# Kernel optimization log

Measured on AMD Instinct MI355X. Metric: run time of the kernel, lower is better.

Reference implementation:

```python
import jax, jax.numpy as jnp
import numpy as np

B, N_ANG, LX, LY, LZ = 2, 120, 128, 128, 128


def _rotate_z(vol, phi):
    """Rotate vol [B,Lx,Ly,Lz] by phi radians (counterclockwise) in the (x,y)
    plane about the grid center, bilinear interpolation, zero padding.
    Mirrors pytomography's rotate_detector_z (bilinear grid-sample rotate)."""
    Lx, Ly = vol.shape[1], vol.shape[2]
    dt = vol.dtype
    cx = (Lx - 1) / 2.0
    cy = (Ly - 1) / 2.0
    xs = jnp.arange(Lx, dtype=dt) - cx
    ys = jnp.arange(Ly, dtype=dt) - cy
    X, Y = jnp.meshgrid(xs, ys, indexing="ij")  # [Lx,Ly]
    c, s = jnp.cos(phi), jnp.sin(phi)
    # inverse rotation maps each output pixel to its source location
    sx = c * X + s * Y + cx
    sy = -s * X + c * Y + cy
    x0 = jnp.floor(sx)
    y0 = jnp.floor(sy)
    wx = (sx - x0)[None, :, :, None]
    wy = (sy - y0)[None, :, :, None]
    x0i = x0.astype(jnp.int32)
    y0i = y0.astype(jnp.int32)

    def gather(xi, yi):
        valid = (xi >= 0) & (xi < Lx) & (yi >= 0) & (yi < Ly)
        xic = jnp.clip(xi, 0, Lx - 1)
        yic = jnp.clip(yi, 0, Ly - 1)
        v = vol[:, xic, yic, :]  # [B,Lx,Ly,Lz]
        return v * valid.astype(dt)[None, :, :, None]

    v00 = gather(x0i, y0i)
    v01 = gather(x0i, y0i + 1)
    v10 = gather(x0i + 1, y0i)
    v11 = gather(x0i + 1, y0i + 1)
    return (v00 * (1 - wx) * (1 - wy) + v01 * (1 - wx) * wy
            + v10 * wx * (1 - wy) + v11 * wx * wy)


def setup_inputs() -> dict:
    key = jax.random.key(0)
    image = jax.random.uniform(key, (B, N_ANG, LY, LZ), dtype=jnp.float32)
    angles = jnp.linspace(0.0, 360.0, N_ANG, endpoint=False).astype(jnp.float32)
    return {"image": image, "angles": angles}


def reference(image, angles, delta=1e-11):
    # image: [B, N_angles, Lr, Lz]; angles in degrees.
    Bn, Na, Lr, Lz = image.shape
    Lx = Ly = Lr
    dt = image.dtype
    phis = -jnp.deg2rad(angles).astype(dt)  # negative=True -> back-rotation

    def step(carry, inp):
        obj_acc, norm_acc = carry
        proj, phi = inp  # proj: [B, Lr, Lz]
        # image[:, i].unsqueeze(1) * ones([B, Lx, Ly, Lz]): broadcast along x
        obj_i = jnp.broadcast_to(proj[:, None, :, :], (Bn, Lx, Ly, Lz))
        norm_i = jnp.ones((Bn, Lx, Ly, Lz), dt)
        obj_acc = obj_acc + _rotate_z(obj_i, phi)
        norm_acc = norm_acc + _rotate_z(norm_i, phi)
        return (obj_acc, norm_acc), None

    init = (jnp.zeros((Bn, Lx, Ly, Lz), dt), jnp.zeros((Bn, Lx, Ly, Lz), dt))
    (obj, norm), _ = jax.lax.scan(step, init, (jnp.swapaxes(image, 0, 1), phis))
    return obj / (norm + jnp.asarray(delta, dt))
```

## Files before the change

kernel.cpp:

```cpp
#include <hip/hip_runtime.h>

namespace {

constexpr int L     = 128;
constexpr int NANG  = 120;
constexpr int CHUNK = 60;
constexpr size_t H16_BYTES = (size_t)2 * NANG * L * L * 2;

typedef __fp16 f16x2 __attribute__((ext_vector_type(2)));
typedef __fp16 f16x4 __attribute__((ext_vector_type(4)));
typedef float  f32x4 __attribute__((ext_vector_type(4)));

__global__ __launch_bounds__(256) void cvt16_kernel(const float* __restrict__ in,
                                                    unsigned* __restrict__ out) {
    const int i = ((int)blockIdx.x * 256 + (int)threadIdx.x) * 4;
    const float4 v = *reinterpret_cast<const float4*>(in + i);
    f16x2 a = __builtin_amdgcn_cvt_pkrtz(v.x, v.y);
    f16x2 b = __builtin_amdgcn_cvt_pkrtz(v.z, v.w);
    uint2 st;
    st.x = *reinterpret_cast<unsigned*>(&a);
    st.y = *reinterpret_cast<unsigned*>(&b);
    *reinterpret_cast<uint2*>(out + i / 2) = st;
}

template <bool F16>
__global__ __launch_bounds__(1024, 4) void bp_kernel(
    const void* __restrict__ imgv,
    const float* __restrict__ angles,
    float* __restrict__ out)
{
    constexpr unsigned SLICE = F16 ? 32768u : 65536u;
    constexpr unsigned ROWB  = F16 ? 256u  : 512u;
    constexpr int      RSH   = F16 ? 8 : 9;

    __shared__ unsigned long long aftab[CHUNK * 4 * 64];
    __shared__ float2   acs[NANG];
    __shared__ unsigned arloB[NANG];
    __shared__ alignas(16) float nrmtab[64];

    const int tid = threadIdx.x;
    const int bid = (int)blockIdx.x;
    const int n   = ((bid & 7) << 5) | (bid >> 3);
    int xt = 0, yt = 0;
#pragma unroll
    for (int i = 0; i < 4; ++i) {
        xt |= ((n >> (2 * i)) & 1) << i;
        yt |= ((n >> (2 * i + 1)) & 1) << i;
    }
    const int xb = xt * 8, yb = yt * 8;
    const float cx = (L - 1) * 0.5f;

    if (tid < NANG) {
        const float phi = -angles[tid] * 0.017453292519943295f;
        float s, c;
        sincosf(phi, &s, &c);
        const float X0 = (float)xb - cx,  X1 = (float)(xb + 7) - cx;
        const float Y0 = (float)yb - cx,  Y1 = (float)(yb + 7) - cx;
        const float a00 = -s * X0 + c * Y0 + cx;
        const float a01 = -s * X0 + c * Y1 + cx;
        const float a10 = -s * X1 + c * Y0 + cx;
        const float a11 = -s * X1 + c * Y1 + cx;
        const float symin = fminf(fminf(a00, a01), fminf(a10, a11));
        acs[tid]   = make_float2(c, s);
        arloB[tid] = (unsigned)min(max((int)floorf(symin), 0), 116) << RSH;
    }
    if (tid < 64) nrmtab[tid] = 0.f;
    __syncthreads();

    const int wave  = tid >> 6;
    const int lane  = tid & 63;
    const int quad  = lane >> 4;
    const int lhalf = lane & 15;
    const int zq    = wave & 3;
    const int b     = (wave >> 2) & 1;
    const int aset  = wave >> 3;
    const char* __restrict__ imgc = (const char*)imgv;

    const unsigned bbase_s = __builtin_amdgcn_readfirstlane((unsigned)(b * NANG) * SLICE);
    const unsigned voffc = (unsigned)((quad == 3) ? 0 : quad) * 4u * ROWB
                         + (unsigned)(zq * 32 + 2 * lhalf) * (F16 ? 2u : 4u);

    auto fill_chunk = [&](int c) {
#pragma unroll
        for (int k = 0; k < 15; ++k) {
            const int e  = tid + k * 1024;
            const int ln = e & 63;
            const int m  = (e >> 6) & 3;
            const int ia = e >> 8;
            const int a  = c * CHUNK + ia;
            const int p  = m * 16 + (ln & 15);
            const int qd = ln >> 4;
            const float2 cs = acs[a];
            const int rlo = (int)(arloB[a] >> RSH);
            const float X = (float)(xb + (p >> 3)) - cx;
            const float Y = (float)(yb + (p & 7)) - cx;
            const float sx =  cs.x * X + cs.y * Y + cx;
            const float sy = -cs.y * X + cs.x * Y + cx;
            const float x0f = floorf(sx), y0f = floorf(sy);
            const float wx = sx - x0f,    wy = sy - y0f;
            const int x0 = (int)x0f, y0 = (int)y0f;
            const float mx0 = (x0 >= 0  && x0 <  L)     ? 1.f : 0.f;
            const float mx1 = (x0 >= -1 && x0 <= L - 2) ? 1.f : 0.f;
            const float my0 = (y0 >= 0  && y0 <  L)     ? 1.f : 0.f;
            const float my1 = (y0 >= -1 && y0 <= L - 2) ? 1.f : 0.f;
            const float A   = (1.f - wx) * mx0 + wx * mx1;
            float w0f = (1.f - wy) * my0 * A;
            float w1f = wy * my1 * A;
            const int y0c = min(max(y0, 0), L - 1);
            const int y1c = min(max(y0 + 1, 0), L - 1);
            const int s0  = min(max(y0c - rlo, 0), 11);
            const int s1  = min(max(y1c - rlo, 0), 11);
            if (s0 == s1) { w0f += w1f; w1f = 0.f; }
            f16x2 wh = __builtin_amdgcn_cvt_pkrtz(w0f, w1f);
            const unsigned wbits = *reinterpret_cast<unsigned*>(&wh);
            const unsigned t  = (unsigned)s0 & 3u;
            const int      q0 = s0 >> 2;
            const unsigned long long W = (unsigned long long)wbits << (t * 16u);
            const unsigned long long spill =
                (t == 3u) ? (unsigned long long)(wbits >> 16) : 0ull;
            aftab[e] = (qd == q0) ? W : ((qd == q0 + 1) ? spill : 0ull);
            if (qd == 0) atomicAdd(&nrmtab[p], w0f + w1f);
        }
    };

    f32x4 acc[4][2] = {};

    auto issue = [&](unsigned long long* af, unsigned* r, float2* rf,
                     int i, int c) {
        const int ia = aset + 2 * i;
        const int a  = c * CHUNK + ia;
#pragma unroll
        for (int m = 0; m < 4; ++m)
            af[m] = aftab[ia * 256 + m * 64 + lane];
        const unsigned rlB = __builtin_amdgcn_readfirstlane(arloB[a]);
        const char* pa = imgc + (bbase_s + (unsigned)a * SLICE + rlB);
        if constexpr (F16) {
#pragma unroll
            for (int j = 0; j < 4; ++j)
                r[j] = *(const unsigned*)(pa + (voffc + (unsigned)j * ROWB));
        } else {
#pragma unroll
            for (int j = 0; j < 4; ++j)
                rf[j] = *(const float2*)(pa + (voffc + (unsigned)j * ROWB));
        }
    };
    auto compute = [&](const unsigned long long* af, const unsigned* r,
                       const float2* rf) {
        union { unsigned u[2]; f16x4 v; } B0, B1;
        if constexpr (F16) {
            B0.u[0] = __builtin_amdgcn_perm(r[1], r[0], 0x05040100u);
            B0.u[1] = __builtin_amdgcn_perm(r[3], r[2], 0x05040100u);
            B1.u[0] = __builtin_amdgcn_perm(r[1], r[0], 0x07060302u);
            B1.u[1] = __builtin_amdgcn_perm(r[3], r[2], 0x07060302u);
        } else {
            const f16x2 h0a = __builtin_amdgcn_cvt_pkrtz(rf[0].x, rf[1].x);
            const f16x2 h0b = __builtin_amdgcn_cvt_pkrtz(rf[2].x, rf[3].x);
            const f16x2 h1a = __builtin_amdgcn_cvt_pkrtz(rf[0].y, rf[1].y);
            const f16x2 h1b = __builtin_amdgcn_cvt_pkrtz(rf[2].y, rf[3].y);
            B0.v = f16x4{h0a.x, h0a.y, h0b.x, h0b.y};
            B1.v = f16x4{h1a.x, h1a.y, h1b.x, h1b.y};
        }
#pragma unroll
        for (int m = 0; m < 4; ++m) {
            union { unsigned long long u; f16x4 v; } afu; afu.u = af[m];
            acc[m][0] = __builtin_amdgcn_mfma_f32_16x16x16f16(afu.v, B0.v, acc[m][0], 0, 0, 0);
            acc[m][1] = __builtin_amdgcn_mfma_f32_16x16x16f16(afu.v, B1.v, acc[m][1], 0, 0, 0);
        }
    };

    unsigned long long aA[4], aB[4], aC[4];
    unsigned rA[4], rB[4], rC[4];
    float2   fA[4], fB[4], fC[4];

    for (int c = 0; c < 2; ++c) {
        fill_chunk(c);
        __syncthreads();
        issue(aA, rA, fA, 0, c);
        issue(aB, rB, fB, 1, c);
        for (int i = 0; i < 30; i += 3) {
            if (i + 2 < 30) issue(aC, rC, fC, i + 2, c);
            compute(aA, rA, fA);
            if (i + 3 < 30) issue(aA, rA, fA, i + 3, c);
            compute(aB, rB, fB);
            if (i + 4 < 30) issue(aB, rB, fB, i + 4, c);
            compute(aC, rC, fC);
            __builtin_amdgcn_s_barrier();
        }
        __syncthreads();
    }

    float4* red = reinterpret_cast<float4*>(aftab);
    const int pr = wave & 7;
    if (aset == 1) {
#pragma unroll
        for (int m = 0; m < 4; ++m)
#pragma unroll
            for (int zg = 0; zg < 2; ++zg)
                red[(pr * 8 + m * 2 + zg) * 64 + lane] =
                    make_float4(acc[m][zg][0], acc[m][zg][1],
                                acc[m][zg][2], acc[m][zg][3]);
    }
    __syncthreads();
    if (aset == 0) {
#pragma unroll
        for (int m = 0; m < 4; ++m)
#pragma unroll
            for (int zg = 0; zg < 2; ++zg) {
                const float4 o = red[(pr * 8 + m * 2 + zg) * 64 + lane];
                acc[m][zg][0] += o.x; acc[m][zg][1] += o.y;
                acc[m][zg][2] += o.z; acc[m][zg][3] += o.w;
            }
        const int zb = zq * 32 + 2 * lhalf;
#pragma unroll
        for (int m = 0; m < 4; ++m) {
            const float4 nrm4 = *(const float4*)&nrmtab[m * 16 + quad * 4];
            const float iv[4] = { 1.f / (nrm4.x + 1e-11f), 1.f / (nrm4.y + 1e-11f),
                                  1.f / (nrm4.z + 1e-11f), 1.f / (nrm4.w + 1e-11f) };
#pragma unroll
            for (int r = 0; r < 4; ++r) {
                const int p = m * 16 + quad * 4 + r;
                const int x = xb + (p >> 3);
                const int y = yb + (p & 7);
                const float2 o = make_float2(acc[m][0][r] * iv[r],
                                             acc[m][1][r] * iv[r]);
                *reinterpret_cast<float2*>(
                    &out[(((size_t)(b * L + x)) * L + y) * L + zb]) = o;
            }
        }
    }
}

}

extern "C" void kernel_launch(void* const* d_in, const int* in_sizes, int n_in,
                              void* d_out, int out_size, void* d_ws, size_t ws_size,
                              hipStream_t stream) {
    const float* image  = (const float*)d_in[0];
    const float* angles = (const float*)d_in[1];
    float* out = (float*)d_out;
    (void)in_sizes; (void)n_in; (void)out_size;

    dim3 grid(256);
    if (d_ws != nullptr && ws_size >= H16_BYTES) {
        cvt16_kernel<<<dim3(3840), 256, 0, stream>>>(image, (unsigned*)d_ws);
        bp_kernel<true><<<grid, 1024, 0, stream>>>(d_ws, angles, out);
    } else {
        bp_kernel<false><<<grid, 1024, 0, stream>>>(image, angles, out);
    }
}
```

Baseline: 115.0 us.

## Split z across blocks, halve per-wave M tiles, shrink angle chunks for occupancy

Doubles the grid to 512 blocks by splitting the z dimension into two halves per block. Within a block the waves now split the M (pixel) tiles in half, so each wave holds half as many accumulators. The angle-weight LDS table is filled in chunks of 24 angles over 5 passes instead of 60 over 2, which shrinks shared memory and allows launch bounds of 8 waves per SIMD. The per-iteration s_barrier is also dropped. The trade-off is that weight-table fill and angle trig are duplicated across the two z halves, and there are more chunk syncs.

Measured after the change: 122.5 us. 6.5% more time.

```diff
diff --git a/kernel.cpp b/kernel.cpp
--- a/kernel.cpp
+++ b/kernel.cpp
@@ -4,7 +4,7 @@
 
 constexpr int L     = 128;
 constexpr int NANG  = 120;
-constexpr int CHUNK = 60;
+constexpr int CHUNK = 24;
 constexpr size_t H16_BYTES = (size_t)2 * NANG * L * L * 2;
 
 typedef __fp16 f16x2 __attribute__((ext_vector_type(2)));
@@ -24,7 +24,7 @@
 }
 
 template <bool F16>
-__global__ __launch_bounds__(1024, 4) void bp_kernel(
+__global__ __launch_bounds__(1024, 8) void bp_kernel(
     const void* __restrict__ imgv,
     const float* __restrict__ angles,
     float* __restrict__ out)
@@ -39,13 +39,15 @@
     __shared__ alignas(16) float nrmtab[64];
 
     const int tid = threadIdx.x;
-    const int bid = (int)blockIdx.x;
-    const int n   = ((bid & 7) << 5) | (bid >> 3);
+    const int bid  = (int)blockIdx.x;
+    const int n    = ((bid & 7) << 6) | (bid >> 3);
+    const int zhf  = n & 1;
+    const int tt   = n >> 1;
     int xt = 0, yt = 0;
 #pragma unroll
     for (int i = 0; i < 4; ++i) {
-        xt |= ((n >> (2 * i)) & 1) << i;
-        yt |= ((n >> (2 * i + 1)) & 1) << i;
+        xt |= ((tt >> (2 * i)) & 1) << i;
+        yt |= ((tt >> (2 * i + 1)) & 1) << i;
     }
     const int xb = xt * 8, yb = yt * 8;
     const float cx = (L - 1) * 0.5f;
@@ -71,25 +73,21 @@
     const int lane  = tid & 63;
     const int quad  = lane >> 4;
     const int lhalf = lane & 15;
-    const int zq    = wave & 3;
-    const int b     = (wave >> 2) & 1;
-    const int aset  = wave >> 3;
+    const int zq2   = wave & 1;
+    const int b     = (wave >> 1) & 1;
+    const int aset  = (wave >> 2) & 1;
+    const int mhalf = wave >> 3;
     const char* __restrict__ imgc = (const char*)imgv;
 
     const unsigned bbase_s = __builtin_amdgcn_readfirstlane((unsigned)(b * NANG) * SLICE);
     const unsigned voffc = (unsigned)((quad == 3) ? 0 : quad) * 4u * ROWB
-                         + (unsigned)(zq * 32 + 2 * lhalf) * (F16 ? 2u : 4u);
+        + (unsigned)(zhf * 64 + zq2 * 32 + 2 * lhalf) * (F16 ? 2u : 4u);
 
     auto fill_chunk = [&](int c) {
-#pragma unroll
-        for (int k = 0; k < 15; ++k) {
-            const int e  = tid + k * 1024;
-            const int ln = e & 63;
-            const int m  = (e >> 6) & 3;
-            const int ia = e >> 8;
+        for (int e = tid; e < CHUNK * 64; e += 1024) {
+            const int p  = e & 63;
+            const int ia = e >> 6;
             const int a  = c * CHUNK + ia;
-            const int p  = m * 16 + (ln & 15);
-            const int qd = ln >> 4;
             const float2 cs = acs[a];
             const int rlo = (int)(arloB[a] >> RSH);
             const float X = (float)(xb + (p >> 3)) - cx;
@@ -118,20 +116,24 @@
             const unsigned long long W = (unsigned long long)wbits << (t * 16u);
             const unsigned long long spill =
                 (t == 3u) ? (unsigned long long)(wbits >> 16) : 0ull;
-            aftab[e] = (qd == q0) ? W : ((qd == q0 + 1) ? spill : 0ull);
-            if (qd == 0) atomicAdd(&nrmtab[p], w0f + w1f);
+            const int eb = ia * 256 + (p >> 4) * 64 + (p & 15);
+#pragma unroll
+            for (int qd = 0; qd < 4; ++qd)
+                aftab[eb + qd * 16] =
+                    (qd == q0) ? W : ((qd == q0 + 1) ? spill : 0ull);
+            atomicAdd(&nrmtab[p], w0f + w1f);
         }
     };
 
-    f32x4 acc[4][2] = {};
+    f32x4 acc[2][2] = {};
 
     auto issue = [&](unsigned long long* af, unsigned* r, float2* rf,
                      int i, int c) {
         const int ia = aset + 2 * i;
         const int a  = c * CHUNK + ia;
 #pragma unroll
-        for (int m = 0; m < 4; ++m)
-            af[m] = aftab[ia * 256 + m * 64 + lane];
+        for (int m = 0; m < 2; ++m)
+            af[m] = aftab[ia * 256 + (mhalf * 2 + m) * 64 + lane];
         const unsigned rlB = __builtin_amdgcn_readfirstlane(arloB[a]);
         const char* pa = imgc + (bbase_s + (unsigned)a * SLICE + rlB);
         if constexpr (F16) {
@@ -161,64 +163,64 @@
             B1.v = f16x4{h1a.x, h1a.y, h1b.x, h1b.y};
         }
 #pragma unroll
-        for (int m = 0; m < 4; ++m) {
+        for (int m = 0; m < 2; ++m) {
             union { unsigned long long u; f16x4 v; } afu; afu.u = af[m];
             acc[m][0] = __builtin_amdgcn_mfma_f32_16x16x16f16(afu.v, B0.v, acc[m][0], 0, 0, 0);
             acc[m][1] = __builtin_amdgcn_mfma_f32_16x16x16f16(afu.v, B1.v, acc[m][1], 0, 0, 0);
         }
     };
 
-    unsigned long long aA[4], aB[4], aC[4];
+    unsigned long long aA[2], aB[2], aC[2];
     unsigned rA[4], rB[4], rC[4];
     float2   fA[4], fB[4], fC[4];
 
-    for (int c = 0; c < 2; ++c) {
+    for (int c = 0; c < 5; ++c) {
         fill_chunk(c);
         __syncthreads();
         issue(aA, rA, fA, 0, c);
         issue(aB, rB, fB, 1, c);
-        for (int i = 0; i < 30; i += 3) {
-            if (i + 2 < 30) issue(aC, rC, fC, i + 2, c);
+        for (int i = 0; i < 12; i += 3) {
+            if (i + 2 < 12) issue(aC, rC, fC, i + 2, c);
             compute(aA, rA, fA);
-            if (i + 3 < 30) issue(aA, rA, fA, i + 3, c);
+            if (i + 3 < 12) issue(aA, rA, fA, i + 3, c);
             compute(aB, rB, fB);
-            if (i + 4 < 30) issue(aB, rB, fB, i + 4, c);
+            if (i + 4 < 12) issue(aB, rB, fB, i + 4, c);
             compute(aC, rC, fC);
-            __builtin_amdgcn_s_barrier();
         }
         __syncthreads();
     }
 
     float4* red = reinterpret_cast<float4*>(aftab);
-    const int pr = wave & 7;
+    const int pr = (zq2 << 2) | (b << 1) | mhalf;
     if (aset == 1) {
 #pragma unroll
-        for (int m = 0; m < 4; ++m)
+        for (int m = 0; m < 2; ++m)
 #pragma unroll
             for (int zg = 0; zg < 2; ++zg)
-                red[(pr * 8 + m * 2 + zg) * 64 + lane] =
+                red[(pr * 4 + m * 2 + zg) * 64 + lane] =
                     make_float4(acc[m][zg][0], acc[m][zg][1],
                                 acc[m][zg][2], acc[m][zg][3]);
     }
     __syncthreads();
     if (aset == 0) {
 #pragma unroll
-        for (int m = 0; m < 4; ++m)
+        for (int m = 0; m < 2; ++m)
 #pragma unroll
             for (int zg = 0; zg < 2; ++zg) {
-                const float4 o = red[(pr * 8 + m * 2 + zg) * 64 + lane];
+                const float4 o = red[(pr * 4 + m * 2 + zg) * 64 + lane];
                 acc[m][zg][0] += o.x; acc[m][zg][1] += o.y;
                 acc[m][zg][2] += o.z; acc[m][zg][3] += o.w;
             }
-        const int zb = zq * 32 + 2 * lhalf;
-#pragma unroll
-        for (int m = 0; m < 4; ++m) {
-            const float4 nrm4 = *(const float4*)&nrmtab[m * 16 + quad * 4];
+        const int zb = zhf * 64 + zq2 * 32 + 2 * lhalf;
+#pragma unroll
+        for (int m = 0; m < 2; ++m) {
+            const int mm = mhalf * 2 + m;
+            const float4 nrm4 = *(const float4*)&nrmtab[mm * 16 + quad * 4];
             const float iv[4] = { 1.f / (nrm4.x + 1e-11f), 1.f / (nrm4.y + 1e-11f),
                                   1.f / (nrm4.z + 1e-11f), 1.f / (nrm4.w + 1e-11f) };
 #pragma unroll
             for (int r = 0; r < 4; ++r) {
-                const int p = m * 16 + quad * 4 + r;
+                const int p = mm * 16 + quad * 4 + r;
                 const int x = xb + (p >> 3);
                 const int y = yb + (p & 7);
                 const float2 o = make_float2(acc[m][0][r] * iv[r],
@@ -240,7 +242,7 @@
     float* out = (float*)d_out;
     (void)in_sizes; (void)n_in; (void)out_size;
 
-    dim3 grid(256);
+    dim3 grid(512);
     if (d_ws != nullptr && ws_size >= H16_BYTES) {
         cvt16_kernel<<<dim3(3840), 256, 0, stream>>>(image, (unsigned*)d_ws);
         bp_kernel<true><<<grid, 1024, 0, stream>>>(d_ws, angles, out);
```
